# Kernel tuning notes

Measured on AMD Instinct MI355X. Metric: run time of the kernel, lower is better.

The kernel has to match this reference:

```python
import jax, jax.numpy as jnp
import numpy as np

B, N, C, O = 512, 64, 256, 256  # batch graphs, agents(nodes), in_ch, out_ch


def _full_graph_edges(n):
    # PyG-style directed upper-triangular edges (j, i+j+1) + self loops,
    # then GCN symmetric normalization with in-degree computed at col.
    src, dst = np.triu_indices(n, k=1)           # src < dst, matches build_edge_index('full')
    loop = np.arange(n)
    row = np.concatenate([src, loop]).astype(np.int32)   # message source
    col = np.concatenate([dst, loop]).astype(np.int32)   # message target (aggregation)
    deg = np.bincount(col, minlength=n).astype(np.float32)
    dis = 1.0 / np.sqrt(deg)
    norm = (dis[row] * dis[col]).astype(np.float32)
    return jnp.asarray(row), jnp.asarray(col), jnp.asarray(norm)


def setup_inputs() -> dict:
    key = jax.random.key(0)
    k1, k2 = jax.random.split(key, 2)
    x = jax.random.normal(k1, (B, N, C), dtype=jnp.float32)
    W = jax.random.normal(k2, (C, O), dtype=jnp.float32) / np.sqrt(C)
    b = jnp.zeros((O,), dtype=jnp.float32)
    return {"x": x, "W": W, "b": b}


def reference(x, W, b):
    # GCNConv: out = D^-1/2 (A + I) D^-1/2 (X W) + b, then ReLU (module forward).
    n = x.shape[1]
    row, col, norm = _full_graph_edges(n)
    xw = jnp.einsum('bnc,co->bno', x, W)                      # [B, N, O]
    msg = xw[:, row, :] * norm[None, :, None]                 # gather along edges [B, E, O]
    agg = jax.vmap(lambda m: jax.ops.segment_sum(m, col, num_segments=n))(msg)  # scatter-add [B, N, O]
    return jax.nn.relu(agg + b)
```

## Files before the change

kernel.cpp:

```cpp
#include <hip/hip_runtime.h>


#define BATCH 512
#define NNODE 64
#define CIN   256
#define COUT  256

typedef __bf16 bf16x8 __attribute__((ext_vector_type(8)));
typedef float  f32x4  __attribute__((ext_vector_type(4)));

__global__ __launch_bounds__(512, 1) void gcn_fused(
    const float* __restrict__ X,
    const float* __restrict__ W,
    const float* __restrict__ bias,
    float* __restrict__ out)
{
    __shared__ uint4 Xs4[2][2048];
    const int tid  = threadIdx.x;
    const int lane = tid & 63;
    const int w    = tid >> 6;
    const int g    = lane >> 4;
    const int c    = lane & 15;
    const int colbase = w * 32;
    const int xg   = blockIdx.x * 2;

    const float* xb0 = X + (size_t)xg * (NNODE * CIN);
    const float* xb1 = xb0 + NNODE * CIN;

    f32x4 pf[8];
#pragma unroll
    for (int i = 0; i < 4; ++i) {
        int ch  = tid + i * 512;
        const f32x4* p = reinterpret_cast<const f32x4*>(
            xb0 + (ch >> 5) * CIN + ((ch & 31) << 3));
        pf[2 * i]     = p[0];
        pf[2 * i + 1] = p[1];
    }

    bf16x8 bfr[8][2];
    {
        const float* Wp = W + colbase + c;
#pragma unroll
        for (int kk = 0; kk < 8; ++kk)
#pragma unroll
            for (int nt = 0; nt < 2; ++nt) {
                bf16x8 t;
#pragma unroll
                for (int j = 0; j < 8; ++j)
                    t[j] = (__bf16)Wp[(size_t)(kk * 32 + g * 8 + j) * COUT + nt * 16];
                bfr[kk][nt] = t;
            }
    }
    float bias_c[2];
#pragma unroll
    for (int nt = 0; nt < 2; ++nt)
        bias_c[nt] = bias[colbase + nt * 16 + c];

#pragma unroll
    for (int i = 0; i < 4; ++i) {
        int ch  = tid + i * 512;
        int row = ch >> 5;
        int c8  = (ch & 31) << 3;
        f32x4 v0 = pf[2 * i], v1 = pf[2 * i + 1];
        bf16x8 h;
        h[0] = (__bf16)v0[0]; h[1] = (__bf16)v0[1];
        h[2] = (__bf16)v0[2]; h[3] = (__bf16)v0[3];
        h[4] = (__bf16)v1[0]; h[5] = (__bf16)v1[1];
        h[6] = (__bf16)v1[2]; h[7] = (__bf16)v1[3];
        int byte = (row << 9) + (c8 << 1);
        byte ^= (row & 7) << 4;
        *reinterpret_cast<uint4*>((unsigned char*)Xs4[0] + byte) =
            __builtin_bit_cast(uint4, h);
    }

    float dd[4][4];
#pragma unroll
    for (int mt = 0; mt < 4; ++mt)
#pragma unroll
        for (int r = 0; r < 4; ++r)
            dd[mt][r] = rsqrtf((float)(mt * 16 + g * 4 + r + 1));

    const int swz = (c & 7) << 4;

    auto compute_graph = [&](const unsigned char* Xs, float* ob) {
        f32x4 acc[4][2] = {};
#pragma unroll
        for (int kk = 0; kk < 8; ++kk) {
            bf16x8 a[4];
#pragma unroll
            for (int mt = 0; mt < 4; ++mt) {
                int byte = ((mt * 16 + c) << 9) + (kk << 6) + (g << 4);
                byte ^= swz;
                a[mt] = *reinterpret_cast<const bf16x8*>(Xs + byte);
            }
#pragma unroll
            for (int mt = 0; mt < 4; ++mt)
#pragma unroll
                for (int nt = 0; nt < 2; ++nt)
                    acc[mt][nt] = __builtin_amdgcn_mfma_f32_16x16x32_bf16(
                        a[mt], bfr[kk][nt], acc[mt][nt], 0, 0, 0);
        }
        float t_[4][2];
#pragma unroll
        for (int mt = 0; mt < 4; ++mt)
#pragma unroll
            for (int nt = 0; nt < 2; ++nt) {
                f32x4 v = acc[mt][nt];
                v[0] *= dd[mt][0]; v[1] *= dd[mt][1];
                v[2] *= dd[mt][2]; v[3] *= dd[mt][3];
                v[1] += v[0]; v[2] += v[1]; v[3] += v[2];
                acc[mt][nt] = v;
                t_[mt][nt] = v[3];
            }
        float Ofs[4][2];
#pragma unroll
        for (int nt = 0; nt < 2; ++nt) {
            float run = 0.0f;
#pragma unroll
            for (int mt = 0; mt < 4; ++mt) {
                float v    = t_[mt][nt];
                float p    = __shfl_xor(v, 16, 64);
                float excl = (g & 1) ? p : 0.0f;
                float pair = v + p;
                float q    = __shfl_xor(pair, 32, 64);
                excl += (g & 2) ? q : 0.0f;
                Ofs[mt][nt] = run + excl;
                run += pair + q;
            }
        }
#pragma unroll
        for (int mt = 0; mt < 4; ++mt)
#pragma unroll
            for (int r = 0; r < 4; ++r) {
                const int row = mt * 16 + g * 4 + r;
                const float dr = dd[mt][r];
#pragma unroll
                for (int nt = 0; nt < 2; ++nt) {
                    float val = (acc[mt][nt][r] + Ofs[mt][nt]) * dr + bias_c[nt];
                    ob[row * COUT + nt * 16] = fmaxf(val, 0.0f);
                }
            }
    };

    __syncthreads();

    f32x4 pg[8];
#pragma unroll
    for (int i = 0; i < 4; ++i) {
        int ch  = tid + i * 512;
        const f32x4* p = reinterpret_cast<const f32x4*>(
            xb1 + (ch >> 5) * CIN + ((ch & 31) << 3));
        pg[2 * i]     = p[0];
        pg[2 * i + 1] = p[1];
    }

    compute_graph((const unsigned char*)Xs4[0],
                  out + (size_t)xg * (NNODE * COUT) + colbase + c);

#pragma unroll
    for (int i = 0; i < 4; ++i) {
        int ch  = tid + i * 512;
        int row = ch >> 5;
        int c8  = (ch & 31) << 3;
        f32x4 v0 = pg[2 * i], v1 = pg[2 * i + 1];
        bf16x8 h;
        h[0] = (__bf16)v0[0]; h[1] = (__bf16)v0[1];
        h[2] = (__bf16)v0[2]; h[3] = (__bf16)v0[3];
        h[4] = (__bf16)v1[0]; h[5] = (__bf16)v1[1];
        h[6] = (__bf16)v1[2]; h[7] = (__bf16)v1[3];
        int byte = (row << 9) + (c8 << 1);
        byte ^= (row & 7) << 4;
        *reinterpret_cast<uint4*>((unsigned char*)Xs4[1] + byte) =
            __builtin_bit_cast(uint4, h);
    }
    __syncthreads();
    compute_graph((const unsigned char*)Xs4[1],
                  out + (size_t)(xg + 1) * (NNODE * COUT) + colbase + c);
}

extern "C" void kernel_launch(void* const* d_in, const int* in_sizes, int n_in,
                              void* d_out, int out_size, void* d_ws, size_t ws_size,
                              hipStream_t stream) {
    const float* x = (const float*)d_in[0];
    const float* W = (const float*)d_in[1];
    const float* bsp = (const float*)d_in[2];
    float* out = (float*)d_out;

    hipLaunchKernelGGL(gcn_fused, dim3(BATCH / 2), dim3(512), 0, stream,
                       x, W, bsp, out);
}
```

Baseline: 20.19 us.

## Process one graph per 256-thread block with 64 output columns per wave

Changes the work split from 256 blocks of 512 threads handling two graphs each (with software-pipelined prefetch of the second graph) to 512 blocks of 256 threads handling one graph each. Each wave now covers 64 output columns with 16 accumulator tiles instead of 32 columns with 8. The aim is more blocks across CUs and a single LDS buffer, with more W register fragments loaded per thread. In exchange it drops the overlap of the second graph's load with the first graph's compute, raises register pressure, and doubles how often W is reloaded in total.

```diff
diff --git a/kernel.cpp b/kernel.cpp
--- a/kernel.cpp
+++ b/kernel.cpp
@@ -9,41 +9,39 @@
 typedef __bf16 bf16x8 __attribute__((ext_vector_type(8)));
 typedef float  f32x4  __attribute__((ext_vector_type(4)));
 
-__global__ __launch_bounds__(512, 1) void gcn_fused(
+__global__ __launch_bounds__(256, 1) void gcn_fused(
     const float* __restrict__ X,
     const float* __restrict__ W,
     const float* __restrict__ bias,
     float* __restrict__ out)
 {
-    __shared__ uint4 Xs4[2][2048];
+    __shared__ uint4 Xs4[2048];
     const int tid  = threadIdx.x;
     const int lane = tid & 63;
     const int w    = tid >> 6;
     const int g    = lane >> 4;
     const int c    = lane & 15;
-    const int colbase = w * 32;
-    const int xg   = blockIdx.x * 2;
+    const int b    = blockIdx.x;
 
-    const float* xb0 = X + (size_t)xg * (NNODE * CIN);
-    const float* xb1 = xb0 + NNODE * CIN;
+    const float* xb = X + (size_t)b * (NNODE * CIN);
 
-    f32x4 pf[8];
+    f32x4 pf[16];
 #pragma unroll
-    for (int i = 0; i < 4; ++i) {
-        int ch  = tid + i * 512;
+    for (int i = 0; i < 8; ++i) {
+        int ch = tid + i * 256;
         const f32x4* p = reinterpret_cast<const f32x4*>(
-            xb0 + (ch >> 5) * CIN + ((ch & 31) << 3));
+            xb + (ch >> 5) * CIN + ((ch & 31) << 3));
         pf[2 * i]     = p[0];
         pf[2 * i + 1] = p[1];
     }
 
-    bf16x8 bfr[8][2];
+    bf16x8 bfr[8][4];
     {
-        const float* Wp = W + colbase + c;
+        const float* Wp = W + w * 64 + c;
 #pragma unroll
         for (int kk = 0; kk < 8; ++kk)
 #pragma unroll
-            for (int nt = 0; nt < 2; ++nt) {
+            for (int nt = 0; nt < 4; ++nt) {
                 bf16x8 t;
 #pragma unroll
                 for (int j = 0; j < 8; ++j)
@@ -51,14 +49,21 @@
                 bfr[kk][nt] = t;
             }
     }
-    float bias_c[2];
+    float bias_c[4];
 #pragma unroll
-    for (int nt = 0; nt < 2; ++nt)
-        bias_c[nt] = bias[colbase + nt * 16 + c];
+    for (int nt = 0; nt < 4; ++nt)
+        bias_c[nt] = bias[w * 64 + nt * 16 + c];
+
+    float dd[4][4];
+#pragma unroll
+    for (int mt = 0; mt < 4; ++mt)
+#pragma unroll
+        for (int r = 0; r < 4; ++r)
+            dd[mt][r] = rsqrtf((float)(mt * 16 + g * 4 + r + 1));
 
 #pragma unroll
-    for (int i = 0; i < 4; ++i) {
-        int ch  = tid + i * 512;
+    for (int i = 0; i < 8; ++i) {
+        int ch  = tid + i * 256;
         int row = ch >> 5;
         int c8  = (ch & 31) << 3;
         f32x4 v0 = pf[2 * i], v1 = pf[2 * i + 1];
@@ -69,113 +74,73 @@
         h[6] = (__bf16)v1[2]; h[7] = (__bf16)v1[3];
         int byte = (row << 9) + (c8 << 1);
         byte ^= (row & 7) << 4;
-        *reinterpret_cast<uint4*>((unsigned char*)Xs4[0] + byte) =
+        *reinterpret_cast<uint4*>((unsigned char*)Xs4 + byte) =
             __builtin_bit_cast(uint4, h);
     }
 
-    float dd[4][4];
+    __syncthreads();
+
+    f32x4 acc[4][4] = {};
+    const int swz = (c & 7) << 4;
 #pragma unroll
-    for (int mt = 0; mt < 4; ++mt)
+    for (int kk = 0; kk < 8; ++kk) {
+        bf16x8 a[4];
 #pragma unroll
-        for (int r = 0; r < 4; ++r)
-            dd[mt][r] = rsqrtf((float)(mt * 16 + g * 4 + r + 1));
-
-    const int swz = (c & 7) << 4;
-
-    auto compute_graph = [&](const unsigned char* Xs, float* ob) {
-        f32x4 acc[4][2] = {};
-#pragma unroll
-        for (int kk = 0; kk < 8; ++kk) {
-            bf16x8 a[4];
-#pragma unroll
-            for (int mt = 0; mt < 4; ++mt) {
-                int byte = ((mt * 16 + c) << 9) + (kk << 6) + (g << 4);
-                byte ^= swz;
-                a[mt] = *reinterpret_cast<const bf16x8*>(Xs + byte);
-            }
-#pragma unroll
-            for (int mt = 0; mt < 4; ++mt)
-#pragma unroll
-                for (int nt = 0; nt < 2; ++nt)
-                    acc[mt][nt] = __builtin_amdgcn_mfma_f32_16x16x32_bf16(
-                        a[mt], bfr[kk][nt], acc[mt][nt], 0, 0, 0);
-        }
-        float t_[4][2];
-#pragma unroll
-        for (int mt = 0; mt < 4; ++mt)
-#pragma unroll
-            for (int nt = 0; nt < 2; ++nt) {
-                f32x4 v = acc[mt][nt];
-                v[0] *= dd[mt][0]; v[1] *= dd[mt][1];
-                v[2] *= dd[mt][2]; v[3] *= dd[mt][3];
-                v[1] += v[0]; v[2] += v[1]; v[3] += v[2];
-                acc[mt][nt] = v;
-                t_[mt][nt] = v[3];
-            }
-        float Ofs[4][2];
-#pragma unroll
-        for (int nt = 0; nt < 2; ++nt) {
-            float run = 0.0f;
-#pragma unroll
-            for (int mt = 0; mt < 4; ++mt) {
-                float v    = t_[mt][nt];
-                float p    = __shfl_xor(v, 16, 64);
-                float excl = (g & 1) ? p : 0.0f;
-                float pair = v + p;
-                float q    = __shfl_xor(pair, 32, 64);
-                excl += (g & 2) ? q : 0.0f;
-                Ofs[mt][nt] = run + excl;
-                run += pair + q;
-            }
+        for (int mt = 0; mt < 4; ++mt) {
+            int byte = ((mt * 16 + c) << 9) + (kk << 6) + (g << 4);
+            byte ^= swz;
+            a[mt] = *reinterpret_cast<const bf16x8*>((const unsigned char*)Xs4 + byte);
         }
 #pragma unroll
         for (int mt = 0; mt < 4; ++mt)
 #pragma unroll
-            for (int r = 0; r < 4; ++r) {
-                const int row = mt * 16 + g * 4 + r;
-                const float dr = dd[mt][r];
-#pragma unroll
-                for (int nt = 0; nt < 2; ++nt) {
-                    float val = (acc[mt][nt][r] + Ofs[mt][nt]) * dr + bias_c[nt];
-                    ob[row * COUT + nt * 16] = fmaxf(val, 0.0f);
-                }
-            }
-    };
-
-    __syncthreads();
-
-    f32x4 pg[8];
-#pragma unroll
-    for (int i = 0; i < 4; ++i) {
-        int ch  = tid + i * 512;
-        const f32x4* p = reinterpret_cast<const f32x4*>(
-            xb1 + (ch >> 5) * CIN + ((ch & 31) << 3));
-        pg[2 * i]     = p[0];
-        pg[2 * i + 1] = p[1];
+            for (int nt = 0; nt < 4; ++nt)
+                acc[mt][nt] = __builtin_amdgcn_mfma_f32_16x16x32_bf16(
+                    a[mt], bfr[kk][nt], acc[mt][nt], 0, 0, 0);
     }
 
-    compute_graph((const unsigned char*)Xs4[0],
-                  out + (size_t)xg * (NNODE * COUT) + colbase + c);
+    float t_[4][4];
+#pragma unroll
+    for (int mt = 0; mt < 4; ++mt)
+#pragma unroll
+        for (int nt = 0; nt < 4; ++nt) {
+            f32x4 v = acc[mt][nt];
+            v[0] *= dd[mt][0]; v[1] *= dd[mt][1];
+            v[2] *= dd[mt][2]; v[3] *= dd[mt][3];
+            v[1] += v[0]; v[2] += v[1]; v[3] += v[2];
+            acc[mt][nt] = v;
+            t_[mt][nt] = v[3];
+        }
+    float Ofs[4][4];
+#pragma unroll
+    for (int nt = 0; nt < 4; ++nt) {
+        float run = 0.0f;
+#pragma unroll
+        for (int mt = 0; mt < 4; ++mt) {
+            float v    = t_[mt][nt];
+            float p    = __shfl_xor(v, 16, 64);
+            float excl = (g & 1) ? p : 0.0f;
+            float pair = v + p;
+            float q    = __shfl_xor(pair, 32, 64);
+            excl += (g & 2) ? q : 0.0f;
+            Ofs[mt][nt] = run + excl;
+            run += pair + q;
+        }
+    }
 
+    float* ob = out + (size_t)b * (NNODE * COUT) + w * 64 + c;
 #pragma unroll
-    for (int i = 0; i < 4; ++i) {
-        int ch  = tid + i * 512;
-        int row = ch >> 5;
-        int c8  = (ch & 31) << 3;
-        f32x4 v0 = pg[2 * i], v1 = pg[2 * i + 1];
-        bf16x8 h;
-        h[0] = (__bf16)v0[0]; h[1] = (__bf16)v0[1];
-        h[2] = (__bf16)v0[2]; h[3] = (__bf16)v0[3];
-        h[4] = (__bf16)v1[0]; h[5] = (__bf16)v1[1];
-        h[6] = (__bf16)v1[2]; h[7] = (__bf16)v1[3];
-        int byte = (row << 9) + (c8 << 1);
-        byte ^= (row & 7) << 4;
-        *reinterpret_cast<uint4*>((unsigned char*)Xs4[1] + byte) =
-            __builtin_bit_cast(uint4, h);
-    }
-    __syncthreads();
-    compute_graph((const unsigned char*)Xs4[1],
-                  out + (size_t)(xg + 1) * (NNODE * COUT) + colbase + c);
+    for (int mt = 0; mt < 4; ++mt)
+#pragma unroll
+        for (int r = 0; r < 4; ++r) {
+            const int row = mt * 16 + g * 4 + r;
+            const float dr = dd[mt][r];
+#pragma unroll
+            for (int nt = 0; nt < 4; ++nt) {
+                float val = (acc[mt][nt][r] + Ofs[mt][nt]) * dr + bias_c[nt];
+                ob[row * COUT + nt * 16] = fmaxf(val, 0.0f);
+            }
+        }
 }
 
 extern "C" void kernel_launch(void* const* d_in, const int* in_sizes, int n_in,
@@ -186,6 +151,6 @@
     const float* bsp = (const float*)d_in[2];
     float* out = (float*)d_out;
 
-    hipLaunchKernelGGL(gcn_fused, dim3(BATCH / 2), dim3(512), 0, stream,
+    hipLaunchKernelGGL(gcn_fused, dim3(BATCH), dim3(256), 0, stream,
                        x, W, bsp, out);
 }
```

Result: slower. 31.31 us (+55.1%).
